# Optimization experiments

Hardware: AMD Instinct MI355X
Metric: run time of the kernel (lower is better)

Reference implementation:

```python
import jax, jax.numpy as jnp
import numpy as np

# Model hyper-params (must match init_kwargs)
B, IN = 8192, 1024          # batch, input_size
E = 16                      # expert_num
H1, H2 = 1024, 512          # expert_dims
T = 2                       # num tasks / gates
TOP_K = 4
HD1, HD2, HD3 = 512, 256, 1 # task head dims
INV_SQRT2 = np.float32(1.0 / np.sqrt(2.0))


def _xavier(key, shape):
    fan_in, fan_out = shape[-2], shape[-1]
    std = np.float32(np.sqrt(2.0 / (fan_in + fan_out)))
    return jax.random.normal(key, shape, dtype=jnp.float32) * std


def setup_inputs() -> dict:
    key = jax.random.key(0)
    ks = jax.random.split(key, 10)
    return {
        "x":   jax.random.normal(ks[0], (B, IN), dtype=jnp.float32),
        # experts (stacked over E)
        "We1": _xavier(ks[1], (E, IN, H1)),
        "be1": jnp.zeros((E, H1), dtype=jnp.float32),
        "We2": _xavier(ks[2], (E, H1, H2)),
        "be2": jnp.zeros((E, H2), dtype=jnp.float32),
        # gates / noise (stacked over T), bias-free since gate_dims=[]
        "Wg":  _xavier(ks[3], (T, IN, E)),
        "Wn":  _xavier(ks[4], (T, IN, E)),
        # task heads (stacked over T; both tasks share dims [512,256,1])
        "Wh1": _xavier(ks[5], (T, H2, HD1)),
        "bh1": jnp.zeros((T, HD1), dtype=jnp.float32),
        "Wh2": _xavier(ks[6], (T, HD1, HD2)),
        "bh2": jnp.zeros((T, HD2), dtype=jnp.float32),
        "Wh3": _xavier(ks[7], (T, HD2, HD3)),
        "bh3": jnp.zeros((T, HD3), dtype=jnp.float32),
    }


def reference(x, We1, be1, We2, be2, Wg, Wn, Wh1, bh1, Wh2, bh2, Wh3, bh3):
    # ---- dense all-experts MLP: Linear -> ReLU -> Linear -------------------
    h = jax.nn.relu(jnp.einsum("bi,eih->beh", x, We1) + be1[None])   # [B,E,H1]
    expert_out = jnp.einsum("beh,eho->beo", h, We2) + be2[None]      # [B,E,H2]

    # ---- noisy top-k gating (per task) -------------------------------------
    mean = jnp.einsum("bi,tie->tbe", x, Wg)                          # [T,B,E]
    std = jax.nn.softplus(jnp.einsum("bi,tie->tbe", x, Wn))          # [T,B,E]
    noise = jax.random.normal(jax.random.key(42), mean.shape, mean.dtype)
    noisy = mean + noise * std

    top_vals, _ = jax.lax.top_k(noisy, TOP_K + 1)                    # [T,B,TOP_K+1] desc
    k_largest = top_vals[..., TOP_K - 1:TOP_K]                       # k-th largest
    k_next = top_vals[..., TOP_K:TOP_K + 1]                          # (k+1)-th largest

    routing_logits = jnp.where(noisy < k_largest, -jnp.inf, noisy)
    thr_excl = jnp.where(noisy == k_largest, k_next, k_largest)
    z = (thr_excl - mean) / (std + 1e-9)
    # Phi(-z) = 0.5 * erfc(z / sqrt(2))  (load proxy, not returned by forward)
    gate_prob = 0.5 * jax.scipy.special.erfc(z * INV_SQRT2)          # noqa: F841

    g = jax.nn.softmax(routing_logits, axis=-1)                      # [T,B,E]

    # ---- weighted sum over experts -----------------------------------------
    gate_out = jnp.einsum("tbe,beo->tbo", g, expert_out)             # [T,B,H2]

    # ---- task heads: Linear->ReLU->Linear->ReLU->Linear --------------------
    t1 = jax.nn.relu(jnp.einsum("tbo,toh->tbh", gate_out, Wh1) + bh1[:, None, :])
    t2 = jax.nn.relu(jnp.einsum("tbh,thk->tbk", t1, Wh2) + bh2[:, None, :])
    out = jnp.einsum("tbk,tko->tbo", t2, Wh3) + bh3[:, None, :]      # [T,B,1]
    return (out[0], out[1])
```

## Files before the change

### kernel.cpp

```cpp
#include <hip/hip_runtime.h>

#define AS1 __attribute__((address_space(1)))
#define AS3 __attribute__((address_space(3)))

typedef __bf16 bf16x8 __attribute__((ext_vector_type(8)));
typedef float f32x4 __attribute__((ext_vector_type(4)));

__device__ __forceinline__ unsigned short f2bf(float f) {
  unsigned u = __float_as_uint(f);
  u += 0x7FFFu + ((u >> 16) & 1u);
  return (unsigned short)(u >> 16);
}
__device__ __forceinline__ float bf2f(unsigned short u) {
  return __uint_as_float(((unsigned)u) << 16);
}

__device__ __forceinline__ void gl_lds16(const void* g, void* l) {
  __builtin_amdgcn_global_load_lds((const AS1 unsigned int*)g,
                                   (AS3 unsigned int*)l, 16, 0, 0);
}

__device__ __forceinline__ unsigned rotl32(unsigned v, int s) {
  return (v << s) | (v >> (32 - s));
}
__device__ __forceinline__ void threefry2x32(unsigned k0, unsigned k1,
                                             unsigned x0, unsigned x1,
                                             unsigned& o0, unsigned& o1) {
  const unsigned ks2 = k0 ^ k1 ^ 0x1BD11BDAu;
  x0 += k0; x1 += k1;
  x0 += x1; x1 = rotl32(x1, 13); x1 ^= x0;
  x0 += x1; x1 = rotl32(x1, 15); x1 ^= x0;
  x0 += x1; x1 = rotl32(x1, 26); x1 ^= x0;
  x0 += x1; x1 = rotl32(x1, 6);  x1 ^= x0;
  x0 += k1; x1 += ks2 + 1u;
  x0 += x1; x1 = rotl32(x1, 17); x1 ^= x0;
  x0 += x1; x1 = rotl32(x1, 29); x1 ^= x0;
  x0 += x1; x1 = rotl32(x1, 16); x1 ^= x0;
  x0 += x1; x1 = rotl32(x1, 24); x1 ^= x0;
  x0 += ks2; x1 += k0 + 2u;
  x0 += x1; x1 = rotl32(x1, 13); x1 ^= x0;
  x0 += x1; x1 = rotl32(x1, 15); x1 ^= x0;
  x0 += x1; x1 = rotl32(x1, 26); x1 ^= x0;
  x0 += x1; x1 = rotl32(x1, 6);  x1 ^= x0;
  x0 += k0; x1 += k1 + 3u;
  x0 += x1; x1 = rotl32(x1, 17); x1 ^= x0;
  x0 += x1; x1 = rotl32(x1, 29); x1 ^= x0;
  x0 += x1; x1 = rotl32(x1, 16); x1 ^= x0;
  x0 += x1; x1 = rotl32(x1, 24); x1 ^= x0;
  x0 += k1; x1 += ks2 + 4u;
  x0 += x1; x1 = rotl32(x1, 13); x1 ^= x0;
  x0 += x1; x1 = rotl32(x1, 15); x1 ^= x0;
  x0 += x1; x1 = rotl32(x1, 26); x1 ^= x0;
  x0 += x1; x1 = rotl32(x1, 6);  x1 ^= x0;
  o0 = x0 + ks2; o1 = x1 + k0 + 5u;
}

__device__ __forceinline__ float erfinv32(float x) {
  float w = -log1pf(-x * x);
  float p;
  if (w < 5.f) {
    w = w - 2.5f;
    p = 2.81022636e-08f;
    p = fmaf(p, w, 3.43273939e-07f);
    p = fmaf(p, w, -3.5233877e-06f);
    p = fmaf(p, w, -4.39150654e-06f);
    p = fmaf(p, w, 0.00021858087f);
    p = fmaf(p, w, -0.00125372503f);
    p = fmaf(p, w, -0.00417768164f);
    p = fmaf(p, w, 0.246640727f);
    p = fmaf(p, w, 1.50140941f);
  } else {
    w = sqrtf(w) - 3.f;
    p = -0.000200214257f;
    p = fmaf(p, w, 0.000100950558f);
    p = fmaf(p, w, 0.00134934322f);
    p = fmaf(p, w, -0.00367342844f);
    p = fmaf(p, w, 0.00573950773f);
    p = fmaf(p, w, -0.0076224613f);
    p = fmaf(p, w, 0.00943887047f);
    p = fmaf(p, w, 1.00167406f);
    p = fmaf(p, w, 2.83297682f);
  }
  return p * x;
}

__device__ __forceinline__ float bits_to_normal(unsigned bits) {
  float f = __uint_as_float((bits >> 9) | 0x3f800000u) - 1.0f;
  const float lo = -0.99999994f;
  float u = fmaf(f, 2.0f, lo);
  u = fmaxf(u, lo);
  return 1.41421356f * erfinv32(u);
}

__global__ __launch_bounds__(256) void cvt_x(const float* __restrict__ in,
                                             unsigned short* __restrict__ out) {
  const int i = blockIdx.x * 256 + threadIdx.x;
  const float4 v = ((const float4*)in)[i];
  ushort4 o;
  o.x = f2bf(v.x); o.y = f2bf(v.y); o.z = f2bf(v.z); o.w = f2bf(v.w);
  ((ushort4*)out)[i] = o;
}

__global__ __launch_bounds__(256) void transpose_bf16(
    const float* __restrict__ in, unsigned short* __restrict__ out, int R, int C) {
  __shared__ float tile[32][33];
  const int bz = blockIdx.z;
  in  += (size_t)bz * R * C;
  out += (size_t)bz * R * C;
  const int c0 = blockIdx.x * 32, r0 = blockIdx.y * 32;
  const int tx = threadIdx.x & 31, ty = threadIdx.x >> 5;
#pragma unroll
  for (int i = 0; i < 32; i += 8)
    tile[ty + i][tx] = in[(size_t)(r0 + ty + i) * C + c0 + tx];
  __syncthreads();
#pragma unroll
  for (int i = 0; i < 32; i += 8)
    out[(size_t)(c0 + ty + i) * R + r0 + tx] = f2bf(tile[tx][ty + i]);
}

__global__ __launch_bounds__(256) void gating_kernel(
    const float* __restrict__ x, const float* __restrict__ Wg,
    const float* __restrict__ Wn, float* __restrict__ g) {
  __shared__ float xs[8][1024];
  __shared__ float partial[64][4][8];
  __shared__ float meanS[2][8][16];
  __shared__ float stdS[2][8][16];
  __shared__ float noisyS[2][8][16];
  const int tid = threadIdx.x;
  const int b0 = blockIdx.x * 8;
  for (int idx = tid; idx < 8 * 1024; idx += 256) {
    int r = idx >> 10, c = idx & 1023;
    xs[r][c] = x[(size_t)(b0 + r) * 1024 + c];
  }
  __syncthreads();
  {
    const int c = tid & 63;
    const int q = tid >> 6;
    const int t = c >> 5, which = (c >> 4) & 1, e = c & 15;
    const float* Wcol = (which ? Wn : Wg) + (size_t)t * 1024 * 16 + e;
    float acc[8] = {0, 0, 0, 0, 0, 0, 0, 0};
    const int i0 = q * 256;
    for (int i = i0; i < i0 + 256; ++i) {
      float w = Wcol[(size_t)i * 16];
#pragma unroll
      for (int r = 0; r < 8; ++r) acc[r] = fmaf(w, xs[r][i], acc[r]);
    }
#pragma unroll
    for (int r = 0; r < 8; ++r) partial[c][q][r] = acc[r];
  }
  __syncthreads();
  for (int idx = tid; idx < 512; idx += 256) {
    int c = idx >> 3, r = idx & 7;
    float s = partial[c][0][r] + partial[c][1][r] + partial[c][2][r] + partial[c][3][r];
    int t = c >> 5, which = (c >> 4) & 1, e = c & 15;
    if (which)
      stdS[t][r][e] = fmaxf(s, 0.f) + log1pf(expf(-fabsf(s)));
    else
      meanS[t][r][e] = s;
  }
  __syncthreads();
  if (tid < 128) {
    int r = tid >> 4, e = tid & 15;
    unsigned p = (unsigned)((b0 + r) * 16 + e);
#pragma unroll
    for (int t = 0; t < 2; ++t) {
      unsigned n = (unsigned)t * 131072u + p;
      unsigned y0, y1;
      threefry2x32(0u, 42u, 0u, n, y0, y1);
      float nrm = bits_to_normal(y0 ^ y1);
      noisyS[t][r][e] = meanS[t][r][e] + nrm * stdS[t][r][e];
    }
  }
  __syncthreads();
  if (tid < 16) {
    int r = tid >> 1, t = tid & 1;
    float v[16];
#pragma unroll
    for (int e = 0; e < 16; ++e) v[e] = noisyS[t][r][e];
    float m0 = -1e30f, m1 = -1e30f, m2 = -1e30f, m3 = -1e30f;
#pragma unroll
    for (int e = 0; e < 16; ++e) {
      float val = v[e];
      if (val > m0) { m3 = m2; m2 = m1; m1 = m0; m0 = val; }
      else if (val > m1) { m3 = m2; m2 = m1; m1 = val; }
      else if (val > m2) { m3 = m2; m2 = val; }
      else if (val > m3) { m3 = val; }
    }
    float sum = 0.f, ge[16];
#pragma unroll
    for (int e = 0; e < 16; ++e) {
      if (v[e] >= m3) { ge[e] = expf(v[e] - m0); sum += ge[e]; }
      else ge[e] = 0.f;
    }
    float inv = 1.f / sum;
    float* grow = g + ((size_t)t * 8192 + (b0 + r)) * 16;
#pragma unroll
    for (int e = 0; e < 16; ++e) grow[e] = ge[e] * inv;
  }
}

__global__ __launch_bounds__(256) void zero_counts(int* __restrict__ counts,
                                                   int n) {
  const int i = blockIdx.x * 256 + threadIdx.x;
  if (i < n) counts[i] = 0;
}

__global__ __launch_bounds__(256) void build_lists(
    const float* __restrict__ g, int Bc, int* __restrict__ counts,
    int* __restrict__ lists, int* __restrict__ slotmap) {
  const int b = blockIdx.x * 256 + threadIdx.x;
  const int lane = threadIdx.x & 63;
  const int chunk = b / Bc, bl = b % Bc;
  float v0[16], v1[16];
  {
    const float4* p0 = (const float4*)(g + (size_t)b * 16);
    const float4* p1 = (const float4*)(g + ((size_t)8192 + b) * 16);
#pragma unroll
    for (int i = 0; i < 4; ++i) {
      ((float4*)v0)[i] = p0[i];
      ((float4*)v1)[i] = p1[i];
    }
  }
  int* cnt = counts + chunk * 16;
  int* lst = lists + (size_t)chunk * 16 * Bc;
  int* smp = slotmap + (size_t)chunk * 16 * Bc;
#pragma unroll
  for (int e = 0; e < 16; ++e) {
    const bool want = (v0[e] != 0.f) || (v1[e] != 0.f);
    const unsigned long long mask = __ballot(want);
    int base = 0;
    if (lane == 0) base = atomicAdd(&cnt[e], (int)__popcll(mask));
    base = __shfl(base, 0, 64);
    if (want) {
      const int slot = base + (int)__popcll(mask & ((1ULL << lane) - 1ULL));
      if (slot < Bc) {
        lst[e * Bc + slot] = b;
        smp[e * Bc + bl] = slot;
      }
    }
  }
}

__global__ __launch_bounds__(64) void build_work(
    const int* __restrict__ counts, int* __restrict__ work,
    int* __restrict__ totals, int gm1, int Bc) {
  const int chunk = blockIdx.x;
  if (threadIdx.x != 0) return;
  const int* cnt = counts + chunk * 16;
  int* w = work + chunk * gm1 * 16;
  int s = 0;
  for (int e = 0; e < 16; ++e) {
    int c = cnt[e];
    if (c < 0) c = 0;
    if (c > Bc) c = Bc;
    const int nt = (c + 127) >> 7;
    for (int t = 0; t < nt; ++t) w[s + t] = (e << 8) | t;
    s += nt;
  }
  totals[chunk] = s;
}

__global__ __launch_bounds__(256) void gather_rows(
    const unsigned short* __restrict__ xb, const int* __restrict__ counts,
    const int* __restrict__ lists, unsigned short* __restrict__ xg, int Bc) {
  const int e = blockIdx.y;
  const int slot = blockIdx.x * 4 + (threadIdx.x >> 6);
  const int lane = threadIdx.x & 63;
  if (slot >= counts[e]) return;
  const int r = lists[(size_t)e * Bc + slot] & 8191;
  const float4* src = (const float4*)(xb + (size_t)r * 1024);
  float4* dst = (float4*)(xg + ((size_t)e * Bc + slot) * 1024);
  dst[lane] = src[lane];
  dst[lane + 64] = src[lane + 64];
}

#define GEMM_DBUF_LOOP()                                                      \
  for (int k0 = 0; k0 < K; k0 += 32) {                                        \
    const int cur = (k0 >> 5) & 1;                                            \
    if (k0 + 32 < K) {                                                        \
      const int nxt = cur ^ 1;                                                \
      gl_lds16(gA0 + k0 + 32, &As[nxt][lofsA0]);                              \
      gl_lds16(gA1 + k0 + 32, &As[nxt][lofsA1]);                              \
      gl_lds16(gB0 + k0 + 32, &Bs[nxt][lofsA0]);                              \
      gl_lds16(gB1 + k0 + 32, &Bs[nxt][lofsA1]);                              \
    }                                                                         \
    bf16x8 af[4], bfr[4];                                                     \
    _Pragma("unroll")                                                         \
    for (int mt = 0; mt < 4; ++mt)                                            \
      af[mt] = *(const bf16x8*)&As[cur][(wm * 64 + mt * 16 + frow) * 32 + fk];\
    _Pragma("unroll")                                                         \
    for (int nt = 0; nt < 4; ++nt)                                            \
      bfr[nt] = *(const bf16x8*)&Bs[cur][(wn * 64 + nt * 16 + frow) * 32 + fk];\
    _Pragma("unroll")                                                         \
    for (int mt = 0; mt < 4; ++mt)                                            \
      _Pragma("unroll")                                                       \
      for (int nt = 0; nt < 4; ++nt)                                          \
        acc[mt][nt] = __builtin_amdgcn_mfma_f32_16x16x32_bf16(                \
            af[mt], bfr[nt], acc[mt][nt], 0, 0, 0);                           \
    __syncthreads();                                                          \
  }

template <bool RELU, bool OUT_BF16>
__global__ __launch_bounds__(256) void gemm_bt(
    const unsigned short* __restrict__ A, int lda, long long strideA,
    const unsigned short* __restrict__ Bt, int ldb, long long strideB,
    void* __restrict__ Cv, int ldc, long long strideC,
    const float* __restrict__ bias, int strideBias, int K,
    int gm, int gn) {
  __shared__ __align__(16) unsigned short As[2][128 * 32];
  __shared__ __align__(16) unsigned short Bs[2][128 * 32];
  const int tid = threadIdx.x;
  const int w = tid >> 6, lane = tid & 63;
  const int wm = w >> 1, wn = w & 1;

  int swz = blockIdx.x;
  const int nwg = gridDim.x;
  if ((nwg & 7) == 0) swz = (swz & 7) * (nwg >> 3) + (swz >> 3);
  const int bm = swz % gm;
  const int tmp = swz / gm;
  const int bn = tmp % gn;
  const int bz = tmp / gn;

  const unsigned short* Ab = A + (size_t)bz * strideA + (size_t)bm * 128 * lda;
  const unsigned short* Bb = Bt + (size_t)bz * strideB + (size_t)bn * 128 * ldb;

  const int srow = lane >> 2;
  const int scol = (lane & 3) * 8;
  const unsigned short* gA0 = Ab + (size_t)(w * 32 + srow) * lda + scol;
  const unsigned short* gA1 = gA0 + (size_t)16 * lda;
  const unsigned short* gB0 = Bb + (size_t)(w * 32 + srow) * ldb + scol;
  const unsigned short* gB1 = gB0 + (size_t)16 * ldb;
  const int lofsA0 = (w * 32) * 32;
  const int lofsA1 = (w * 32 + 16) * 32;

  f32x4 acc[4][4] = {};
  const int frow = lane & 15;
  const int fk = (lane >> 4) * 8;

  gl_lds16(gA0, &As[0][lofsA0]);
  gl_lds16(gA1, &As[0][lofsA1]);
  gl_lds16(gB0, &Bs[0][lofsA0]);
  gl_lds16(gB1, &Bs[0][lofsA1]);
  __syncthreads();

  GEMM_DBUF_LOOP()

  const int crow = (lane >> 4) * 4;
  const int ccol = lane & 15;
  const float* brow = bias + (size_t)bz * strideBias + (size_t)bn * 128;
#pragma unroll
  for (int nt = 0; nt < 4; ++nt) {
    int col = wn * 64 + nt * 16 + ccol;
    float bv = brow[col];
#pragma unroll
    for (int mt = 0; mt < 4; ++mt) {
      f32x4 v = acc[mt][nt];
#pragma unroll
      for (int r = 0; r < 4; ++r) {
        float val = v[r] + bv;
        if (RELU) val = fmaxf(val, 0.f);
        size_t row = (size_t)bm * 128 + wm * 64 + mt * 16 + crow + r;
        size_t off = (size_t)bz * strideC + row * ldc + (size_t)bn * 128 + col;
        if (OUT_BF16) ((unsigned short*)Cv)[off] = f2bf(val);
        else          ((float*)Cv)[off] = val;
      }
    }
  }
}

template <bool RELU>
__global__ __launch_bounds__(256) void gemm_sparse(
    const unsigned short* __restrict__ A, int lda, long long strideA,
    const unsigned short* __restrict__ Bt, int ldb, long long strideB,
    unsigned short* __restrict__ C, int ldc, long long strideC,
    const float* __restrict__ bias, int strideBias, int K,
    const int* __restrict__ counts, const int* __restrict__ work,
    const int* __restrict__ totalp, int lgn, int gm1, int Bc) {
  __shared__ __align__(16) unsigned short As[2][128 * 32];
  __shared__ __align__(16) unsigned short Bs[2][128 * 32];
  const int tid = threadIdx.x;
  const int w = tid >> 6, lane = tid & 63;
  const int wm = w >> 1, wn = w & 1;

  int T = (*totalp) << lgn;
  const int nwg = gridDim.x;
  if (T > nwg) T = nwg;
  const int j = blockIdx.x;
  const int x = j & 7, rank = j >> 3;
  const int q = T >> 3, r = T & 7;
  const int quota = q + (x < r ? 1 : 0);
  if (rank >= quota) return;
  const int i = (x < r ? x * (q + 1) : r * (q + 1) + (x - r) * q) + rank;
  const int tile = i >> lgn, bn = i & ((1 << lgn) - 1);
  const int wentry = work[tile];
  const int bz = (wentry >> 8) & 15;
  const int bm = wentry & (gm1 - 1);
  int mcount = counts[bz];
  if (mcount > Bc) mcount = Bc;
  if (mcount < 0) mcount = 0;

  const unsigned short* Ab = A + (size_t)bz * strideA + (size_t)bm * 128 * lda;
  const unsigned short* Bb = Bt + (size_t)bz * strideB + (size_t)bn * 128 * ldb;

  const int srow = lane >> 2;
  const int scol = (lane & 3) * 8;
  const unsigned short* gA0 = Ab + (size_t)(w * 32 + srow) * lda + scol;
  const unsigned short* gA1 = gA0 + (size_t)16 * lda;
  const unsigned short* gB0 = Bb + (size_t)(w * 32 + srow) * ldb + scol;
  const unsigned short* gB1 = gB0 + (size_t)16 * ldb;
  const int lofsA0 = (w * 32) * 32;
  const int lofsA1 = (w * 32 + 16) * 32;

  f32x4 acc[4][4] = {};
  const int frow = lane & 15;
  const int fk = (lane >> 4) * 8;

  gl_lds16(gA0, &As[0][lofsA0]);
  gl_lds16(gA1, &As[0][lofsA1]);
  gl_lds16(gB0, &Bs[0][lofsA0]);
  gl_lds16(gB1, &Bs[0][lofsA1]);
  __syncthreads();

  GEMM_DBUF_LOOP()

  const int crow = (lane >> 4) * 4;
  const int ccol = lane & 15;
  const float* brow = bias + (size_t)bz * strideBias + (size_t)bn * 128;
#pragma unroll
  for (int nt = 0; nt < 4; ++nt) {
    int col = wn * 64 + nt * 16 + ccol;
    float bv = brow[col];
#pragma unroll
    for (int mt = 0; mt < 4; ++mt) {
      f32x4 v = acc[mt][nt];
#pragma unroll
      for (int r = 0; r < 4; ++r) {
        float val = v[r] + bv;
        if (RELU) val = fmaxf(val, 0.f);
        int row = bm * 128 + wm * 64 + mt * 16 + crow + r;
        if (row < mcount) {
          size_t off = (size_t)bz * strideC + (size_t)row * ldc +
                       (size_t)bn * 128 + col;
          C[off] = f2bf(val);
        }
      }
    }
  }
}

__global__ __launch_bounds__(128) void combine_kernel(
    const unsigned short* __restrict__ eo, const float* __restrict__ g,
    unsigned short* __restrict__ go, int b0, long long strideE,
    const int* __restrict__ slotmap, int Bc) {
  const int bl = blockIdx.x, t = blockIdx.y;
  const int b = b0 + bl;
  const int o = threadIdx.x;
  const float* grow = g + ((size_t)t * 8192 + b) * 16;
  float a0 = 0, a1 = 0, a2 = 0, a3 = 0;
  for (int e = 0; e < 16; ++e) {
    float ge = grow[e];
    if (ge != 0.f) {
      const int slot = slotmap[e * Bc + bl] & (Bc - 1);
      const unsigned short* row = eo + (size_t)e * strideE + (size_t)slot * 512;
      a0 = fmaf(ge, bf2f(row[o]), a0);
      a1 = fmaf(ge, bf2f(row[o + 128]), a1);
      a2 = fmaf(ge, bf2f(row[o + 256]), a2);
      a3 = fmaf(ge, bf2f(row[o + 384]), a3);
    }
  }
  unsigned short* orow = go + ((size_t)t * 8192 + b) * 512;
  orow[o] = f2bf(a0); orow[o + 128] = f2bf(a1);
  orow[o + 256] = f2bf(a2); orow[o + 384] = f2bf(a3);
}

__global__ __launch_bounds__(256) void final_dot(const float* __restrict__ t2,
                                                 const float* __restrict__ Wh3,
                                                 const float* __restrict__ bh3,
                                                 float* __restrict__ out) {
  const int row = blockIdx.x * 4 + (threadIdx.x >> 6);
  const int lane = threadIdx.x & 63;
  const int t = row >> 13;
  const float* trow = t2 + (size_t)row * 256;
  const float* w = Wh3 + t * 256;
  float s = 0.f;
#pragma unroll
  for (int j = 0; j < 4; ++j) s = fmaf(trow[lane + j * 64], w[lane + j * 64], s);
#pragma unroll
  for (int off = 32; off > 0; off >>= 1) s += __shfl_down(s, off, 64);
  if (lane == 0) out[row] = s + bh3[t];
}

extern "C" void kernel_launch(void* const* d_in, const int* in_sizes, int n_in,
                              void* d_out, int out_size, void* d_ws, size_t ws_size,
                              hipStream_t stream) {
  (void)in_sizes; (void)n_in; (void)out_size;
  const float* x   = (const float*)d_in[0];
  const float* We1 = (const float*)d_in[1];
  const float* be1 = (const float*)d_in[2];
  const float* We2 = (const float*)d_in[3];
  const float* be2 = (const float*)d_in[4];
  const float* Wg  = (const float*)d_in[5];
  const float* Wn  = (const float*)d_in[6];
  const float* Wh1 = (const float*)d_in[7];
  const float* bh1 = (const float*)d_in[8];
  const float* Wh2 = (const float*)d_in[9];
  const float* bh2 = (const float*)d_in[10];
  const float* Wh3 = (const float*)d_in[11];
  const float* bh3 = (const float*)d_in[12];

  auto al = [](size_t v) { return (v + 255) & ~(size_t)255; };
  const size_t sz_xb   = al((size_t)8192 * 1024 * 2);
  const size_t sz_We1t = al((size_t)16 * 1024 * 1024 * 2);
  const size_t sz_We2t = al((size_t)16 * 512 * 1024 * 2);
  const size_t sz_Wh1t = al((size_t)2 * 512 * 512 * 2);
  const size_t sz_Wh2t = al((size_t)2 * 256 * 512 * 2);
  const size_t sz_g    = al((size_t)2 * 8192 * 16 * 4);
  const size_t sz_go   = al((size_t)2 * 8192 * 512 * 2);
  const size_t sz_cnt  = al((size_t)8 * 16 * 4);
  const size_t sz_lst  = al((size_t)16 * 8192 * 4);
  const size_t sz_smp  = al((size_t)16 * 8192 * 4);
  const size_t sz_wrk  = al((size_t)1024 * 4);
  const size_t sz_tot  = al((size_t)8 * 4);
  const size_t fixed = sz_xb + sz_We1t + sz_We2t + sz_Wh1t + sz_Wh2t + sz_g +
                       sz_go + sz_cnt + sz_lst + sz_smp + sz_wrk + sz_tot;
  const size_t sz_t1 = al((size_t)2 * 8192 * 512 * 2);
  const size_t sz_t2 = al((size_t)2 * 8192 * 256 * 4);
  const size_t sz_t12 = sz_t1 + sz_t2;

  int Bc = 1024;
  {
    const int cands[4] = {8192, 4096, 2048, 1024};
    for (int ci = 0; ci < 4; ++ci) {
      int c = cands[ci];
      size_t region = 2 * al((size_t)16 * c * 1024 * 2);
      if (region < sz_t12) region = sz_t12;
      if (fixed + region <= ws_size) { Bc = c; break; }
    }
  }
  const size_t sz_hc = al((size_t)16 * Bc * 1024 * 2);
  const int nchunk = 8192 / Bc;
  const int gm1 = Bc / 128;

  char* ws = (char*)d_ws;
  size_t off = 0;
  auto carve = [&](size_t bytes) -> char* { char* p = ws + off; off += bytes; return p; };
  unsigned short* xb   = (unsigned short*)carve(sz_xb);
  unsigned short* We1t = (unsigned short*)carve(sz_We1t);
  unsigned short* We2t = (unsigned short*)carve(sz_We2t);
  unsigned short* Wh1t = (unsigned short*)carve(sz_Wh1t);
  unsigned short* Wh2t = (unsigned short*)carve(sz_Wh2t);
  float* g             = (float*)carve(sz_g);
  unsigned short* go   = (unsigned short*)carve(sz_go);
  int* counts          = (int*)carve(sz_cnt);
  int* lists           = (int*)carve(sz_lst);
  int* slotmap         = (int*)carve(sz_smp);
  int* work            = (int*)carve(sz_wrk);
  int* totals          = (int*)carve(sz_tot);
  char* region         = ws + off;
  unsigned short* xg   = (unsigned short*)region;
  unsigned short* eo   = (unsigned short*)region;
  unsigned short* h    = (unsigned short*)(region + sz_hc);
  unsigned short* t1   = (unsigned short*)region;
  float* t2            = (float*)(region + sz_t1);

  cvt_x<<<8192, 256, 0, stream>>>(x, xb);
  transpose_bf16<<<dim3(32, 32, 16), 256, 0, stream>>>(We1, We1t, 1024, 1024);
  transpose_bf16<<<dim3(16, 32, 16), 256, 0, stream>>>(We2, We2t, 1024, 512);
  transpose_bf16<<<dim3(16, 16, 2), 256, 0, stream>>>(Wh1, Wh1t, 512, 512);
  transpose_bf16<<<dim3(8, 16, 2), 256, 0, stream>>>(Wh2, Wh2t, 512, 256);

  gating_kernel<<<1024, 256, 0, stream>>>(x, Wg, Wn, g);
  zero_counts<<<1, 256, 0, stream>>>(counts, nchunk * 16);
  build_lists<<<32, 256, 0, stream>>>(g, Bc, counts, lists, slotmap);
  build_work<<<nchunk, 64, 0, stream>>>(counts, work, totals, gm1, Bc);

  for (int b0 = 0; b0 < 8192; b0 += Bc) {
    const int chunk = b0 / Bc;
    const int* cnt = counts + chunk * 16;
    const int* lst = lists + (size_t)chunk * 16 * Bc;
    const int* smp = slotmap + (size_t)chunk * 16 * Bc;
    const int* wrk = work + chunk * gm1 * 16;
    const int* tot = totals + chunk;
    gather_rows<<<dim3(Bc / 4, 16), 256, 0, stream>>>(xb, cnt, lst, xg, Bc);
    gemm_sparse<true><<<gm1 * 16 * 8, 256, 0, stream>>>(
        xg, 1024, (long long)Bc * 1024,
        We1t, 1024, (long long)1024 * 1024,
        h, 1024, (long long)Bc * 1024, be1, 1024, 1024,
        cnt, wrk, tot, 3, gm1, Bc);
    gemm_sparse<false><<<gm1 * 16 * 4, 256, 0, stream>>>(
        h, 1024, (long long)Bc * 1024,
        We2t, 1024, (long long)512 * 1024,
        eo, 512, (long long)Bc * 512, be2, 512, 1024,
        cnt, wrk, tot, 2, gm1, Bc);
    combine_kernel<<<dim3(Bc, 2), 128, 0, stream>>>(
        eo, g, go, b0, (long long)Bc * 512, smp, Bc);
  }

  gemm_bt<true, true><<<64 * 4 * 2, 256, 0, stream>>>(
      go, 512, (long long)8192 * 512, Wh1t, 512, (long long)512 * 512,
      t1, 512, (long long)8192 * 512, bh1, 512, 512,
      64, 4);
  gemm_bt<true, false><<<64 * 2 * 2, 256, 0, stream>>>(
      t1, 512, (long long)8192 * 512, Wh2t, 512, (long long)256 * 512,
      t2, 256, (long long)8192 * 256, bh2, 256, 512,
      64, 2);

  final_dot<<<4096, 256, 0, stream>>>(t2, Wh3, bh3, (float*)d_out);
}
```

Measured before the change: 766.7 us.

## Use triple-buffered LDS pipeline with vmcnt waits in GEMM kernels

Replaces the double-buffered K loop in the dense and sparse GEMM kernels with a three-stage LDS ring. Loads run two steps ahead, and each step waits with explicit s_waitcnt vmcnt plus a single barrier instead of a trailing __syncthreads. The aim is to hide more global-load latency and drop one barrier per iteration. The cost is 50% more LDS per block (48KB), which may lower occupancy, and the hand-written vmcnt counting has to stay exact for the result to be correct.

```diff
diff --git a/kernel.cpp b/kernel.cpp
--- a/kernel.cpp
+++ b/kernel.cpp
@@ -274,15 +274,20 @@
   dst[lane + 64] = src[lane + 64];
 }
 
-#define GEMM_DBUF_LOOP()                                                      \
+#define GEMM_PIPE3_LOOP()                                                     \
   for (int k0 = 0; k0 < K; k0 += 32) {                                        \
-    const int cur = (k0 >> 5) & 1;                                            \
-    if (k0 + 32 < K) {                                                        \
-      const int nxt = cur ^ 1;                                                \
-      gl_lds16(gA0 + k0 + 32, &As[nxt][lofsA0]);                              \
-      gl_lds16(gA1 + k0 + 32, &As[nxt][lofsA1]);                              \
-      gl_lds16(gB0 + k0 + 32, &Bs[nxt][lofsA0]);                              \
-      gl_lds16(gB1 + k0 + 32, &Bs[nxt][lofsA1]);                              \
+    const int step = k0 >> 5;                                                 \
+    const int cur = step % 3;                                                 \
+    if (k0 + 32 < K) asm volatile("s_waitcnt vmcnt(4)" ::: "memory");         \
+    else             asm volatile("s_waitcnt vmcnt(0)" ::: "memory");         \
+    __builtin_amdgcn_s_barrier();                                             \
+    asm volatile("" ::: "memory");                                            \
+    if (k0 + 64 < K) {                                                        \
+      const int pf = cur == 0 ? 2 : cur - 1;                  \
+      gl_lds16(gA0 + k0 + 64, &As[pf][lofsA0]);                               \
+      gl_lds16(gA1 + k0 + 64, &As[pf][lofsA1]);                               \
+      gl_lds16(gB0 + k0 + 64, &Bs[pf][lofsA0]);                               \
+      gl_lds16(gB1 + k0 + 64, &Bs[pf][lofsA1]);                               \
     }                                                                         \
     bf16x8 af[4], bfr[4];                                                     \
     _Pragma("unroll")                                                         \
@@ -297,7 +302,18 @@
       for (int nt = 0; nt < 4; ++nt)                                          \
         acc[mt][nt] = __builtin_amdgcn_mfma_f32_16x16x32_bf16(                \
             af[mt], bfr[nt], acc[mt][nt], 0, 0, 0);                           \
-    __syncthreads();                                                          \
+  }
+
+#define GEMM_PIPE3_PROLOGUE()                                                 \
+  gl_lds16(gA0, &As[0][lofsA0]);                                              \
+  gl_lds16(gA1, &As[0][lofsA1]);                                              \
+  gl_lds16(gB0, &Bs[0][lofsA0]);                                              \
+  gl_lds16(gB1, &Bs[0][lofsA1]);                                              \
+  if (K > 32) {                                                               \
+    gl_lds16(gA0 + 32, &As[1][lofsA0]);                                       \
+    gl_lds16(gA1 + 32, &As[1][lofsA1]);                                       \
+    gl_lds16(gB0 + 32, &Bs[1][lofsA0]);                                       \
+    gl_lds16(gB1 + 32, &Bs[1][lofsA1]);                                       \
   }
 
 template <bool RELU, bool OUT_BF16>
@@ -307,8 +323,8 @@
     void* __restrict__ Cv, int ldc, long long strideC,
     const float* __restrict__ bias, int strideBias, int K,
     int gm, int gn) {
-  __shared__ __align__(16) unsigned short As[2][128 * 32];
-  __shared__ __align__(16) unsigned short Bs[2][128 * 32];
+  __shared__ __align__(16) unsigned short As[3][128 * 32];
+  __shared__ __align__(16) unsigned short Bs[3][128 * 32];
   const int tid = threadIdx.x;
   const int w = tid >> 6, lane = tid & 63;
   const int wm = w >> 1, wn = w & 1;
@@ -337,13 +353,8 @@
   const int frow = lane & 15;
   const int fk = (lane >> 4) * 8;
 
-  gl_lds16(gA0, &As[0][lofsA0]);
-  gl_lds16(gA1, &As[0][lofsA1]);
-  gl_lds16(gB0, &Bs[0][lofsA0]);
-  gl_lds16(gB1, &Bs[0][lofsA1]);
-  __syncthreads();
-
-  GEMM_DBUF_LOOP()
+  GEMM_PIPE3_PROLOGUE()
+  GEMM_PIPE3_LOOP()
 
   const int crow = (lane >> 4) * 4;
   const int ccol = lane & 15;
@@ -376,8 +387,8 @@
     const float* __restrict__ bias, int strideBias, int K,
     const int* __restrict__ counts, const int* __restrict__ work,
     const int* __restrict__ totalp, int lgn, int gm1, int Bc) {
-  __shared__ __align__(16) unsigned short As[2][128 * 32];
-  __shared__ __align__(16) unsigned short Bs[2][128 * 32];
+  __shared__ __align__(16) unsigned short As[3][128 * 32];
+  __shared__ __align__(16) unsigned short Bs[3][128 * 32];
   const int tid = threadIdx.x;
   const int w = tid >> 6, lane = tid & 63;
   const int wm = w >> 1, wn = w & 1;
@@ -415,13 +426,8 @@
   const int frow = lane & 15;
   const int fk = (lane >> 4) * 8;
 
-  gl_lds16(gA0, &As[0][lofsA0]);
-  gl_lds16(gA1, &As[0][lofsA1]);
-  gl_lds16(gB0, &Bs[0][lofsA0]);
-  gl_lds16(gB1, &Bs[0][lofsA1]);
-  __syncthreads();
-
-  GEMM_DBUF_LOOP()
+  GEMM_PIPE3_PROLOGUE()
+  GEMM_PIPE3_LOOP()
 
   const int crow = (lane >> 4) * 4;
   const int ccol = lane & 15;
```

Result: no change. 775.0 us (+1.1%).

## Pack per-expert gathered rows contiguously using prefix offsets instead of fixed slots

Applied to the files above, without the earlier changes.

Per-expert activation buffers for xg, h and eo are now packed back to back. Each expert starts at a 128-row-aligned prefix offset computed in build_work, instead of a fixed Bc-row slot per expert. The gather, both sparse GEMMs and the combine kernel use these offsets. The packed region is sized 8*Bc+2048 rows rather than 16*Bc, so a larger batch chunk may fit in the workspace, giving fewer chunk iterations and more GEMM tiles per launch. It also makes the buffers denser. Offsets are clamped so an out-of-range offset stays inside the buffer, which could silently alias rows if the assumption of at most 8 experts per row were broken.

```diff
diff --git a/kernel.cpp b/kernel.cpp
--- a/kernel.cpp
+++ b/kernel.cpp
@@ -243,33 +243,46 @@
 
 __global__ __launch_bounds__(64) void build_work(
     const int* __restrict__ counts, int* __restrict__ work,
-    int* __restrict__ totals, int gm1, int Bc) {
+    int* __restrict__ totals, int* __restrict__ offsets,
+    int gm1, int Bc, int cap) {
   const int chunk = blockIdx.x;
   if (threadIdx.x != 0) return;
   const int* cnt = counts + chunk * 16;
   int* w = work + chunk * gm1 * 16;
+  int* offs = offsets + chunk * 16;
   int s = 0;
+  int rows = 0;
   for (int e = 0; e < 16; ++e) {
     int c = cnt[e];
     if (c < 0) c = 0;
     if (c > Bc) c = Bc;
+    int o = rows;
+    if (o > cap - Bc) o = cap - Bc;
+    offs[e] = o;
     const int nt = (c + 127) >> 7;
     for (int t = 0; t < nt; ++t) w[s + t] = (e << 8) | t;
     s += nt;
+    rows += nt << 7;
   }
   totals[chunk] = s;
 }
 
 __global__ __launch_bounds__(256) void gather_rows(
     const unsigned short* __restrict__ xb, const int* __restrict__ counts,
-    const int* __restrict__ lists, unsigned short* __restrict__ xg, int Bc) {
+    const int* __restrict__ lists, const int* __restrict__ offs,
+    unsigned short* __restrict__ xg, int Bc, int cap) {
   const int e = blockIdx.y;
   const int slot = blockIdx.x * 4 + (threadIdx.x >> 6);
   const int lane = threadIdx.x & 63;
-  if (slot >= counts[e]) return;
+  int c = counts[e];
+  if (c > Bc) c = Bc;
+  if (slot >= c) return;
+  int o = offs[e];
+  if (o < 0) o = 0;
+  if (o > cap - Bc) o = cap - Bc;
   const int r = lists[(size_t)e * Bc + slot] & 8191;
   const float4* src = (const float4*)(xb + (size_t)r * 1024);
-  float4* dst = (float4*)(xg + ((size_t)e * Bc + slot) * 1024);
+  float4* dst = (float4*)(xg + ((size_t)o + slot) * 1024);
   dst[lane] = src[lane];
   dst[lane + 64] = src[lane + 64];
 }
@@ -370,12 +383,13 @@
 
 template <bool RELU>
 __global__ __launch_bounds__(256) void gemm_sparse(
-    const unsigned short* __restrict__ A, int lda, long long strideA,
+    const unsigned short* __restrict__ A, int lda,
     const unsigned short* __restrict__ Bt, int ldb, long long strideB,
-    unsigned short* __restrict__ C, int ldc, long long strideC,
+    unsigned short* __restrict__ C, int ldc,
     const float* __restrict__ bias, int strideBias, int K,
-    const int* __restrict__ counts, const int* __restrict__ work,
-    const int* __restrict__ totalp, int lgn, int gm1, int Bc) {
+    const int* __restrict__ counts, const int* __restrict__ offs,
+    const int* __restrict__ work, const int* __restrict__ totalp,
+    int lgn, int gm1, int Bc, int cap) {
   __shared__ __align__(16) unsigned short As[2][128 * 32];
   __shared__ __align__(16) unsigned short Bs[2][128 * 32];
   const int tid = threadIdx.x;
@@ -398,8 +412,11 @@
   int mcount = counts[bz];
   if (mcount > Bc) mcount = Bc;
   if (mcount < 0) mcount = 0;
-
-  const unsigned short* Ab = A + (size_t)bz * strideA + (size_t)bm * 128 * lda;
+  int offz = offs[bz];
+  if (offz < 0) offz = 0;
+  if (offz > cap - Bc) offz = cap - Bc;
+
+  const unsigned short* Ab = A + (size_t)(offz + bm * 128) * lda;
   const unsigned short* Bb = Bt + (size_t)bz * strideB + (size_t)bn * 128 * ldb;
 
   const int srow = lane >> 2;
@@ -439,8 +456,7 @@
         if (RELU) val = fmaxf(val, 0.f);
         int row = bm * 128 + wm * 64 + mt * 16 + crow + r;
         if (row < mcount) {
-          size_t off = (size_t)bz * strideC + (size_t)row * ldc +
-                       (size_t)bn * 128 + col;
+          size_t off = (size_t)(offz + row) * ldc + (size_t)bn * 128 + col;
           C[off] = f2bf(val);
         }
       }
@@ -450,8 +466,8 @@
 
 __global__ __launch_bounds__(128) void combine_kernel(
     const unsigned short* __restrict__ eo, const float* __restrict__ g,
-    unsigned short* __restrict__ go, int b0, long long strideE,
-    const int* __restrict__ slotmap, int Bc) {
+    unsigned short* __restrict__ go, int b0, const int* __restrict__ offs,
+    const int* __restrict__ slotmap, int Bc, int cap) {
   const int bl = blockIdx.x, t = blockIdx.y;
   const int b = b0 + bl;
   const int o = threadIdx.x;
@@ -461,7 +477,10 @@
     float ge = grow[e];
     if (ge != 0.f) {
       const int slot = slotmap[e * Bc + bl] & (Bc - 1);
-      const unsigned short* row = eo + (size_t)e * strideE + (size_t)slot * 512;
+      int oz = offs[e];
+      if (oz < 0) oz = 0;
+      if (oz > cap - Bc) oz = cap - Bc;
+      const unsigned short* row = eo + (size_t)(oz + slot) * 512;
       a0 = fmaf(ge, bf2f(row[o]), a0);
       a1 = fmaf(ge, bf2f(row[o + 128]), a1);
       a2 = fmaf(ge, bf2f(row[o + 256]), a2);
@@ -521,8 +540,9 @@
   const size_t sz_smp  = al((size_t)16 * 8192 * 4);
   const size_t sz_wrk  = al((size_t)1024 * 4);
   const size_t sz_tot  = al((size_t)8 * 4);
+  const size_t sz_off  = al((size_t)8 * 16 * 4);
   const size_t fixed = sz_xb + sz_We1t + sz_We2t + sz_Wh1t + sz_Wh2t + sz_g +
-                       sz_go + sz_cnt + sz_lst + sz_smp + sz_wrk + sz_tot;
+                       sz_go + sz_cnt + sz_lst + sz_smp + sz_wrk + sz_tot + sz_off;
   const size_t sz_t1 = al((size_t)2 * 8192 * 512 * 2);
   const size_t sz_t2 = al((size_t)2 * 8192 * 256 * 4);
   const size_t sz_t12 = sz_t1 + sz_t2;
@@ -532,12 +552,14 @@
     const int cands[4] = {8192, 4096, 2048, 1024};
     for (int ci = 0; ci < 4; ++ci) {
       int c = cands[ci];
-      size_t region = 2 * al((size_t)16 * c * 1024 * 2);
+      size_t cap_c = (size_t)8 * c + 2048;
+      size_t region = 2 * al(cap_c * 1024 * 2);
       if (region < sz_t12) region = sz_t12;
       if (fixed + region <= ws_size) { Bc = c; break; }
     }
   }
-  const size_t sz_hc = al((size_t)16 * Bc * 1024 * 2);
+  const int cap = 8 * Bc + 2048;
+  const size_t sz_hc = al((size_t)cap * 1024 * 2);
   const int nchunk = 8192 / Bc;
   const int gm1 = Bc / 128;
 
@@ -556,6 +578,7 @@
   int* slotmap         = (int*)carve(sz_smp);
   int* work            = (int*)carve(sz_wrk);
   int* totals          = (int*)carve(sz_tot);
+  int* offsets         = (int*)carve(sz_off);
   char* region         = ws + off;
   unsigned short* xg   = (unsigned short*)region;
   unsigned short* eo   = (unsigned short*)region;
@@ -572,7 +595,7 @@
   gating_kernel<<<1024, 256, 0, stream>>>(x, Wg, Wn, g);
   zero_counts<<<1, 256, 0, stream>>>(counts, nchunk * 16);
   build_lists<<<32, 256, 0, stream>>>(g, Bc, counts, lists, slotmap);
-  build_work<<<nchunk, 64, 0, stream>>>(counts, work, totals, gm1, Bc);
+  build_work<<<nchunk, 64, 0, stream>>>(counts, work, totals, offsets, gm1, Bc, cap);
 
   for (int b0 = 0; b0 < 8192; b0 += Bc) {
     const int chunk = b0 / Bc;
@@ -581,19 +604,20 @@
     const int* smp = slotmap + (size_t)chunk * 16 * Bc;
     const int* wrk = work + chunk * gm1 * 16;
     const int* tot = totals + chunk;
-    gather_rows<<<dim3(Bc / 4, 16), 256, 0, stream>>>(xb, cnt, lst, xg, Bc);
+    const int* ofs = offsets + chunk * 16;
+    gather_rows<<<dim3(Bc / 4, 16), 256, 0, stream>>>(xb, cnt, lst, ofs, xg, Bc, cap);
     gemm_sparse<true><<<gm1 * 16 * 8, 256, 0, stream>>>(
-        xg, 1024, (long long)Bc * 1024,
+        xg, 1024,
         We1t, 1024, (long long)1024 * 1024,
-        h, 1024, (long long)Bc * 1024, be1, 1024, 1024,
-        cnt, wrk, tot, 3, gm1, Bc);
+        h, 1024, be1, 1024, 1024,
+        cnt, ofs, wrk, tot, 3, gm1, Bc, cap);
     gemm_sparse<false><<<gm1 * 16 * 4, 256, 0, stream>>>(
-        h, 1024, (long long)Bc * 1024,
+        h, 1024,
         We2t, 1024, (long long)512 * 1024,
-        eo, 512, (long long)Bc * 512, be2, 512, 1024,
-        cnt, wrk, tot, 2, gm1, Bc);
+        eo, 512, be2, 512, 1024,
+        cnt, ofs, wrk, tot, 2, gm1, Bc, cap);
     combine_kernel<<<dim3(Bc, 2), 128, 0, stream>>>(
-        eo, g, go, b0, (long long)Bc * 512, smp, Bc);
+        eo, g, go, b0, ofs, smp, Bc, cap);
   }
 
   gemm_bt<true, true><<<64 * 4 * 2, 256, 0, stream>>>(
```

Measured after the change: 702.2 us. 1.09x faster.
